# Kernel tuning notes

Hardware: AMD Instinct MI355X
Metric: run time of the kernel (lower is better)

The kernel has to match this reference:

```python
import jax, jax.numpy as jnp
import numpy as np

DIM = 1536
NUM_HEADS = 12
HEAD_DIM = DIM // NUM_HEADS  # 128
EPS = 1e-6


def _rms_norm(x, weight, eps=EPS):
    # x: [B, S, C], computed in float32 like the torch module
    xf = x.astype(jnp.float32)
    xf = xf * jax.lax.rsqrt(jnp.mean(xf * xf, axis=-1, keepdims=True) + eps)
    return (xf * weight).astype(x.dtype)


def _rotate_half(x):
    x1, x2 = jnp.split(x, 2, axis=-1)
    return jnp.concatenate([-x2, x1], axis=-1)


def setup_inputs() -> dict:
    key = jax.random.key(0)
    ks = jax.random.split(key, 12)
    B, S = 1, 4096
    scale = 1.0 / np.sqrt(DIM)
    x = jax.random.normal(ks[0], (B, S, DIM), dtype=jnp.float32)
    # RoPE tables [S, head_dim]
    pos = jnp.arange(S, dtype=jnp.float32)[:, None]
    inv_freq = 1.0 / (10000.0 ** (jnp.arange(0, HEAD_DIM, 2, dtype=jnp.float32) / HEAD_DIM))
    ang = pos * inv_freq[None, :]                      # [S, head_dim/2]
    ang = jnp.concatenate([ang, ang], axis=-1)         # [S, head_dim]
    freqs_cos = jnp.cos(ang)
    freqs_sin = jnp.sin(ang)
    Wq = jax.random.normal(ks[1], (DIM, DIM), dtype=jnp.float32) * scale
    bq = jnp.zeros((DIM,), dtype=jnp.float32)
    Wk = jax.random.normal(ks[2], (DIM, DIM), dtype=jnp.float32) * scale
    bk = jnp.zeros((DIM,), dtype=jnp.float32)
    Wv = jax.random.normal(ks[3], (DIM, DIM), dtype=jnp.float32) * scale
    bv = jnp.zeros((DIM,), dtype=jnp.float32)
    Wo = jax.random.normal(ks[4], (DIM, DIM), dtype=jnp.float32) * scale
    bo = jnp.zeros((DIM,), dtype=jnp.float32)
    gq = jnp.ones((DIM,), dtype=jnp.float32)
    gk = jnp.ones((DIM,), dtype=jnp.float32)
    return {"x": x, "freqs_cos": freqs_cos, "freqs_sin": freqs_sin,
            "Wq": Wq, "bq": bq, "Wk": Wk, "bk": bk, "Wv": Wv, "bv": bv,
            "Wo": Wo, "bo": bo, "gq": gq, "gk": gk}


def reference(x, freqs_cos, freqs_sin, Wq, bq, Wk, bk, Wv, bv, Wo, bo, gq, gk):
    b, s, _ = x.shape
    n, d = NUM_HEADS, HEAD_DIM
    q = _rms_norm(x @ Wq.T + bq, gq).reshape(b, s, n, d)
    k = _rms_norm(x @ Wk.T + bk, gk).reshape(b, s, n, d)
    v = (x @ Wv.T + bv).reshape(b, s, n, d)
    # RoPE: freqs [S, d] -> broadcast over batch and heads
    cos = freqs_cos[None, :, None, :]
    sin = freqs_sin[None, :, None, :]
    q = q * cos + _rotate_half(q) * sin
    k = k * cos + _rotate_half(k) * sin
    # SDPA, non-causal
    scores = jnp.einsum('bqnd,bknd->bnqk', q, k) / jnp.sqrt(jnp.asarray(d, x.dtype))
    attn = jax.nn.softmax(scores, axis=-1)
    out = jnp.einsum('bnqk,bknd->bqnd', attn, v).reshape(b, s, n * d)
    return out @ Wo.T + bo
```

## Files before the change

### kernel.cpp

```cpp
#include <hip/hip_runtime.h>

typedef unsigned short ushort_t;
typedef short bf16x8 __attribute__((ext_vector_type(8)));
typedef float f32x4 __attribute__((ext_vector_type(4)));
typedef float f32x16 __attribute__((ext_vector_type(16)));

#define S_LEN 4096
#define DIM   1536
#define NH    12
#define HD    128
#define KVSPLIT 4
#define ROWS (NH * S_LEN)
#define OPSPLIT_ELEMS ((size_t)ROWS * HD)

__device__ __forceinline__ float bf2f(ushort_t h) {
  union { unsigned u; float f; } v; v.u = ((unsigned)h) << 16; return v.f;
}
__device__ __forceinline__ ushort_t f2bf(float f) {
  union { float f; unsigned u; } v; v.f = f;
  return (ushort_t)((v.u + 0x7FFFu + ((v.u >> 16) & 1u)) >> 16);
}
__device__ __forceinline__ unsigned cvtpk(float lo, float hi_) {
  unsigned r; asm("v_cvt_pk_bf16_f32 %0, %1, %2" : "=v"(r) : "v"(lo), "v"(hi_)); return r;
}

#define GLD16(gp, lp) __builtin_amdgcn_global_load_lds( \
    (const __attribute__((address_space(1))) unsigned int*)(gp), \
    (__attribute__((address_space(3))) unsigned int*)(lp), 16, 0, 0)

__global__ void __launch_bounds__(256) cvt_bf16(const float* __restrict__ in,
                                                ushort_t* __restrict__ out, int n4) {
  int i = blockIdx.x * 256 + threadIdx.x;
  int stride = gridDim.x * 256;
  for (; i < n4; i += stride) {
    float4 v = ((const float4*)in)[i];
    ushort4 o;
    o.x = f2bf(v.x); o.y = f2bf(v.y); o.z = f2bf(v.z); o.w = f2bf(v.w);
    ((ushort4*)out)[i] = o;
  }
}

template <int F32OUT>
__global__ void __launch_bounds__(256) gemm_bt(
    const ushort_t* __restrict__ A, const ushort_t* __restrict__ Wbase,
    const float* __restrict__ b0, const float* __restrict__ b1, const float* __restrict__ b2,
    void* __restrict__ Cbase_v, int M, int N, int K)
{
  const int z = blockIdx.z;
  const ushort_t* W = Wbase + (size_t)z * N * K;
  const float* bias = (z == 0) ? b0 : (z == 1) ? b1 : b2;

  const int n0 = blockIdx.x * 128;
  const int m0 = blockIdx.y * 128;
  const int t = threadIdx.x;
  const int lane = t & 63;
  const int w = t >> 6;
  const int wr = w >> 1, wc = w & 1;
  const int mp = lane & 15, g = lane >> 4;

  __shared__ __attribute__((aligned(16))) ushort_t As[128 * 64];
  __shared__ __attribute__((aligned(16))) ushort_t Bs[128 * 64];

  f32x4 acc[4][4];
  f32x4 zero = {0.f, 0.f, 0.f, 0.f};
#pragma unroll
  for (int i = 0; i < 4; ++i)
#pragma unroll
    for (int j = 0; j < 4; ++j) acc[i][j] = zero;

  for (int kt = 0; kt < K; kt += 64) {
    __syncthreads();
#pragma unroll
    for (int i = 0; i < 4; ++i) {
      int p = i * 256 + t;
      int r = p >> 3, sl = p & 7;
      int sg = sl ^ (r & 7);
      GLD16(A + (size_t)(m0 + r) * K + kt + sg * 8, As + p * 8);
      GLD16(W + (size_t)(n0 + r) * K + kt + sg * 8, Bs + p * 8);
    }
    __syncthreads();
#pragma unroll
    for (int kk = 0; kk < 2; ++kk) {
      bf16x8 af[4], bfr[4];
#pragma unroll
      for (int mi = 0; mi < 4; ++mi) {
        int row = wr * 64 + mi * 16 + mp;
        int ch = (g + 4 * kk) ^ (row & 7);
        af[mi] = *(const bf16x8*)(As + row * 64 + ch * 8);
      }
#pragma unroll
      for (int ni = 0; ni < 4; ++ni) {
        int row = wc * 64 + ni * 16 + mp;
        int ch = (g + 4 * kk) ^ (row & 7);
        bfr[ni] = *(const bf16x8*)(Bs + row * 64 + ch * 8);
      }
#pragma unroll
      for (int mi = 0; mi < 4; ++mi)
#pragma unroll
        for (int ni = 0; ni < 4; ++ni)
          acc[mi][ni] = __builtin_amdgcn_mfma_f32_16x16x32_bf16(af[mi], bfr[ni], acc[mi][ni], 0, 0, 0);
    }
  }
#pragma unroll
  for (int ni = 0; ni < 4; ++ni) {
    int n = n0 + wc * 64 + ni * 16 + mp;
    float bv = bias[n];
#pragma unroll
    for (int mi = 0; mi < 4; ++mi) {
      int mbase = m0 + wr * 64 + mi * 16 + g * 4;
#pragma unroll
      for (int j = 0; j < 4; ++j) {
        if constexpr (F32OUT) {
          ((float*)Cbase_v)[(size_t)z * M * N + (size_t)(mbase + j) * N + n] =
              acc[mi][ni][j] + bv;
        } else {
          ((ushort_t*)Cbase_v)[(size_t)z * M * N + (size_t)(mbase + j) * N + n] =
              f2bf(acc[mi][ni][j] + bv);
        }
      }
    }
  }
}

__global__ void __launch_bounds__(256) epi_qkv(
    const ushort_t* __restrict__ raw,
    const float* __restrict__ gq, const float* __restrict__ gk,
    const float* __restrict__ fcos, const float* __restrict__ fsin,
    ushort_t* __restrict__ Qh, ushort_t* __restrict__ Kh, ushort_t* __restrict__ Vh)
{
  const int s = blockIdx.x;
  const int t = threadIdx.x;
  const ushort_t* rq = raw + (size_t)s * DIM;
  const ushort_t* rk = raw + (size_t)S_LEN * DIM + (size_t)s * DIM;
  const ushort_t* rv = raw + 2 * (size_t)S_LEN * DIM + (size_t)s * DIM;

  float sq = 0.f, sk = 0.f;
#pragma unroll
  for (int i = 0; i < 6; ++i) {
    int e = t + 256 * i;
    float a = bf2f(rq[e]); sq += a * a;
    float b = bf2f(rk[e]); sk += b * b;
  }
  for (int off = 1; off < 64; off <<= 1) {
    sq += __shfl_xor(sq, off, 64);
    sk += __shfl_xor(sk, off, 64);
  }
  __shared__ float red[2][4];
  int w = t >> 6;
  if ((t & 63) == 0) { red[0][w] = sq; red[1][w] = sk; }
  __syncthreads();
  sq = red[0][0] + red[0][1] + red[0][2] + red[0][3];
  sk = red[1][0] + red[1][1] + red[1][2] + red[1][3];
  float invq = rsqrtf(sq * (1.f / 1536.f) + 1e-6f);
  float invk = rsqrtf(sk * (1.f / 1536.f) + 1e-6f);

  const float qscale = 0.12752004708465604f;
#pragma unroll
  for (int i = 0; i < 3; ++i) {
    int p = t + 256 * i;
    int hh = p >> 6, d = p & 63;
    int e1 = hh * 128 + d, e2 = e1 + 64;
    float c1 = fcos[s * 128 + d],      s1 = fsin[s * 128 + d];
    float c2 = fcos[s * 128 + d + 64], s2 = fsin[s * 128 + d + 64];
    float q1 = bf2f(rq[e1]) * invq * gq[e1];
    float q2 = bf2f(rq[e2]) * invq * gq[e2];
    float k1 = bf2f(rk[e1]) * invk * gk[e1];
    float k2 = bf2f(rk[e2]) * invk * gk[e2];
    size_t ob = ((size_t)hh * S_LEN + s) * 128;
    Qh[ob + d]      = f2bf((q1 * c1 - q2 * s1) * qscale);
    Qh[ob + d + 64] = f2bf((q2 * c2 + q1 * s2) * qscale);
    Kh[ob + d]      = f2bf(k1 * c1 - k2 * s1);
    Kh[ob + d + 64] = f2bf(k2 * c2 + k1 * s2);
  }
#pragma unroll
  for (int i = 0; i < 6; ++i) {
    int e = t + 256 * i;
    int hh = e >> 7, d = e & 127;
    Vh[((size_t)hh * S_LEN + s) * 128 + d] = rv[e];
  }
}

__global__ void __launch_bounds__(256) transpose_v(const ushort_t* __restrict__ Vh,
                                                   ushort_t* __restrict__ VT) {
  const int st = blockIdx.x * 64;
  const int dt = blockIdx.y * 64;
  const int h = blockIdx.z;
  __shared__ ushort_t tile[64][65];
  const int t = threadIdx.x;
#pragma unroll
  for (int i = 0; i < 2; ++i) {
    int p = i * 256 + t;
    int r = p >> 3, c = (p & 7) * 8;
    bf16x8 v = *(const bf16x8*)(Vh + ((size_t)h * S_LEN + st + r) * 128 + dt + c);
#pragma unroll
    for (int j = 0; j < 8; ++j) tile[r][c + j] = ((ushort_t*)&v)[j];
  }
  __syncthreads();
#pragma unroll
  for (int i = 0; i < 2; ++i) {
    int p = i * 256 + t;
    int r = p >> 3, c = (p & 7) * 8;
    ushort_t tmp[8];
#pragma unroll
    for (int j = 0; j < 8; ++j) tmp[j] = tile[c + j][r];
    *(bf16x8*)(VT + ((size_t)h * 128 + dt + r) * S_LEN + st + c) = *(bf16x8*)tmp;
  }
}

__device__ __forceinline__ void stage_kv(const ushort_t* __restrict__ Kg,
                                         const ushort_t* __restrict__ Vg,
                                         ushort_t* KsB, ushort_t* VsB, int t) {
#pragma unroll
  for (int i = 0; i < 8; ++i) {
    int p = i * 128 + t;
    int r = p >> 4, sl = p & 15;
    int sg = sl ^ (r & 7);
    GLD16(Kg + (size_t)r * 128 + sg * 8, KsB + p * 8);
  }
#pragma unroll
  for (int i = 0; i < 8; ++i) {
    int p = i * 128 + t;
    int r = p >> 3, sl = p & 7;
    int sg = sl ^ (r & 7);
    GLD16(Vg + (size_t)r * S_LEN + sg * 8, VsB + p * 8);
  }
}

struct AttnState {
  f32x16 oacc[4];
  float mrun, lrun;
};

__device__ __forceinline__ void attn_tile(const ushort_t* KsB, const ushort_t* VsB,
                                          const bf16x8* qf, AttnState& st_,
                                          int ql, int hi) {
  f32x16 sa0, sa1;
#pragma unroll
  for (int r = 0; r < 16; ++r) { sa0[r] = 0.f; sa1[r] = 0.f; }
  __builtin_amdgcn_s_setprio(1);
#pragma unroll
  for (int s = 0; s < 8; ++s) {
    int ck = (2 * s + hi) ^ (ql & 7);
    bf16x8 k0 = *(const bf16x8*)(KsB + ql * 128 + ck * 8);
    bf16x8 k1 = *(const bf16x8*)(KsB + (32 + ql) * 128 + ck * 8);
    sa0 = __builtin_amdgcn_mfma_f32_32x32x16_bf16(k0, qf[s], sa0, 0, 0, 0);
    sa1 = __builtin_amdgcn_mfma_f32_32x32x16_bf16(k1, qf[s], sa1, 0, 0, 0);
  }
  __builtin_amdgcn_s_setprio(0);

  float mt[8];
#pragma unroll
  for (int r = 0; r < 8; ++r)
    mt[r] = fmaxf(fmaxf(sa0[r], sa0[r + 8]), fmaxf(sa1[r], sa1[r + 8]));
#pragma unroll
  for (int off = 4; off > 0; off >>= 1)
#pragma unroll
    for (int r = 0; r < 8; ++r)
      if (r < off) mt[r] = fmaxf(mt[r], mt[r + off]);
  float mx = fmaxf(mt[0], __shfl_xor(mt[0], 32));

  if (__any(mx - st_.mrun > 11.0f)) {
    float nm = fmaxf(st_.mrun, mx);
    float sc = exp2f(st_.mrun - nm);
    st_.mrun = nm;
    st_.lrun *= sc;
#pragma unroll
    for (int dt = 0; dt < 4; ++dt)
#pragma unroll
      for (int r = 0; r < 16; ++r) st_.oacc[dt][r] *= sc;
  }

  float rt[8];
#pragma unroll
  for (int r = 0; r < 16; ++r) {
    sa0[r] = exp2f(sa0[r] - st_.mrun);
    sa1[r] = exp2f(sa1[r] - st_.mrun);
  }
#pragma unroll
  for (int r = 0; r < 8; ++r) rt[r] = (sa0[r] + sa0[r + 8]) + (sa1[r] + sa1[r + 8]);
#pragma unroll
  for (int off = 4; off > 0; off >>= 1)
#pragma unroll
    for (int r = 0; r < 8; ++r)
      if (r < off) rt[r] += rt[r + off];
  st_.lrun += rt[0] + __shfl_xor(rt[0], 32);

  unsigned pw0[8], pw1[8];
#pragma unroll
  for (int a = 0; a < 4; ++a) {
    pw0[2 * a]     = cvtpk(sa0[4 * a], sa0[4 * a + 1]);
    pw0[2 * a + 1] = cvtpk(sa0[4 * a + 2], sa0[4 * a + 3]);
    pw1[2 * a]     = cvtpk(sa1[4 * a], sa1[4 * a + 1]);
    pw1[2 * a + 1] = cvtpk(sa1[4 * a + 2], sa1[4 * a + 3]);
  }

#pragma unroll
  for (int sx = 0; sx < 2; ++sx) {
#pragma unroll
    for (int ks = 0; ks < 2; ++ks) {
      unsigned q0w0 = sx ? pw1[4 * ks + 0] : pw0[4 * ks + 0];
      unsigned q0w1 = sx ? pw1[4 * ks + 1] : pw0[4 * ks + 1];
      unsigned q1w0 = sx ? pw1[4 * ks + 2] : pw0[4 * ks + 2];
      unsigned q1w1 = sx ? pw1[4 * ks + 3] : pw0[4 * ks + 3];
      unsigned sw0 = hi ? q0w0 : q1w0;
      unsigned sw1 = hi ? q0w1 : q1w1;
      unsigned rv0 = (unsigned)__shfl_xor((int)sw0, 32);
      unsigned rv1 = (unsigned)__shfl_xor((int)sw1, 32);
      union { unsigned u[4]; bf16x8 v; } fw;
      fw.u[0] = hi ? rv0 : q0w0;
      fw.u[1] = hi ? rv1 : q0w1;
      fw.u[2] = hi ? q1w0 : rv0;
      fw.u[3] = hi ? q1w1 : rv1;
      __builtin_amdgcn_s_setprio(1);
#pragma unroll
      for (int dt = 0; dt < 4; ++dt) {
        int d = 32 * dt + ql;
        int cv = (4 * sx + 2 * ks + hi) ^ (ql & 7);
        bf16x8 va = *(const bf16x8*)(VsB + d * 64 + cv * 8);
        st_.oacc[dt] = __builtin_amdgcn_mfma_f32_32x32x16_bf16(va, fw.v, st_.oacc[dt], 0, 0, 0);
      }
      __builtin_amdgcn_s_setprio(0);
    }
  }
}

__device__ __forceinline__ void attn_epilogue(AttnState& st_, int z, int row, int hi,
                                              ushort_t* __restrict__ opraw,
                                              ushort_t* __restrict__ opxb,
                                              float* __restrict__ mlbuf) {
  ushort_t* Op = (z < 3) ? (opraw + (size_t)z * OPSPLIT_ELEMS) : opxb;
  float inv = 1.f / st_.lrun;
#pragma unroll
  for (int dt = 0; dt < 4; ++dt) {
#pragma unroll
    for (int c = 0; c < 4; ++c) {
      float f0 = st_.oacc[dt][4 * c + 0] * inv, f1 = st_.oacc[dt][4 * c + 1] * inv;
      float f2 = st_.oacc[dt][4 * c + 2] * inv, f3 = st_.oacc[dt][4 * c + 3] * inv;
      uint2 u;
      u.x = cvtpk(f0, f1);
      u.y = cvtpk(f2, f3);
      *(uint2*)(Op + (size_t)row * 128 + 32 * dt + 8 * c + 4 * hi) = u;
    }
  }
  if (hi == 0) {
    mlbuf[2 * ((size_t)z * ROWS + row)]     = st_.mrun;
    mlbuf[2 * ((size_t)z * ROWS + row) + 1] = st_.lrun;
  }
}

__global__ void __launch_bounds__(128) attn32(
    const ushort_t* __restrict__ Qh, const ushort_t* __restrict__ Kh,
    const ushort_t* __restrict__ VT,
    ushort_t* __restrict__ opraw, ushort_t* __restrict__ opxb,
    float* __restrict__ mlbuf, int zoff)
{
  const int qt = blockIdx.x;
  const int h = blockIdx.y;
  const int z = blockIdx.z + zoff;
  const int t = threadIdx.x;
  const int lane = t & 63;
  const int w = t >> 6;
  const int ql = lane & 31;
  const int hi = lane >> 5;

  __shared__ __attribute__((aligned(16))) ushort_t Ks[64 * 128];
  __shared__ __attribute__((aligned(16))) ushort_t Vs[128 * 64];

  const int q0 = qt * 64 + w * 32;
  const size_t kbase = (size_t)h * S_LEN * 128;
  const size_t vbase = (size_t)h * 128 * S_LEN;

  bf16x8 qf[8];
#pragma unroll
  for (int s = 0; s < 8; ++s)
    qf[s] = *(const bf16x8*)(Qh + ((size_t)h * S_LEN + q0 + ql) * 128 + 16 * s + 8 * hi);

  AttnState st_;
#pragma unroll
  for (int dt = 0; dt < 4; ++dt)
#pragma unroll
    for (int r = 0; r < 16; ++r) st_.oacc[dt][r] = 0.f;
  st_.mrun = -1e30f; st_.lrun = 0.f;

  const int kvbeg = z * (S_LEN / KVSPLIT);
  const int kvend = kvbeg + S_LEN / KVSPLIT;
  for (int kv0 = kvbeg; kv0 < kvend; kv0 += 64) {
    __syncthreads();
    stage_kv(Kh + kbase + (size_t)kv0 * 128, VT + vbase + kv0, Ks, Vs, t);
    __syncthreads();
    attn_tile(Ks, Vs, qf, st_, ql, hi);
  }
  attn_epilogue(st_, z, h * S_LEN + q0 + ql, hi, opraw, opxb, mlbuf);
}

__global__ void __launch_bounds__(128) attn32p(
    const ushort_t* __restrict__ Qh, const ushort_t* __restrict__ Kh,
    const ushort_t* __restrict__ VT,
    ushort_t* __restrict__ opraw, ushort_t* __restrict__ opxb,
    float* __restrict__ mlbuf, int zoff)
{
  const int qt = blockIdx.x;
  const int h = blockIdx.y;
  const int z = blockIdx.z + zoff;
  const int t = threadIdx.x;
  const int lane = t & 63;
  const int w = t >> 6;
  const int ql = lane & 31;
  const int hi = lane >> 5;

  __shared__ __attribute__((aligned(16))) ushort_t Ks[2][64 * 128];
  __shared__ __attribute__((aligned(16))) ushort_t Vs[2][128 * 64];

  const int q0 = qt * 64 + w * 32;
  const size_t kbase = (size_t)h * S_LEN * 128;
  const size_t vbase = (size_t)h * 128 * S_LEN;

  bf16x8 qf[8];
#pragma unroll
  for (int s = 0; s < 8; ++s)
    qf[s] = *(const bf16x8*)(Qh + ((size_t)h * S_LEN + q0 + ql) * 128 + 16 * s + 8 * hi);

  AttnState st_;
#pragma unroll
  for (int dt = 0; dt < 4; ++dt)
#pragma unroll
    for (int r = 0; r < 16; ++r) st_.oacc[dt][r] = 0.f;
  st_.mrun = -1e30f; st_.lrun = 0.f;

  const int kvbeg = z * (S_LEN / KVSPLIT);
  const int NT = (S_LEN / KVSPLIT) / 64;

  stage_kv(Kh + kbase + (size_t)kvbeg * 128, VT + vbase + kvbeg, Ks[0], Vs[0], t);

  for (int it = 0; it < NT; ++it) {
    const int cur = it & 1;
    if (it + 1 < NT) {
      const int kvn = kvbeg + (it + 1) * 64;
      stage_kv(Kh + kbase + (size_t)kvn * 128, VT + vbase + kvn, Ks[cur ^ 1], Vs[cur ^ 1], t);
      asm volatile("s_waitcnt vmcnt(16)" ::: "memory");
    } else {
      asm volatile("s_waitcnt vmcnt(0)" ::: "memory");
    }
    __builtin_amdgcn_sched_barrier(0);
    __builtin_amdgcn_s_barrier();
    __builtin_amdgcn_sched_barrier(0);
    attn_tile(Ks[cur], Vs[cur], qf, st_, ql, hi);
    __builtin_amdgcn_s_barrier();
  }
  attn_epilogue(st_, z, h * S_LEN + q0 + ql, hi, opraw, opxb, mlbuf);
}

__global__ void __launch_bounds__(256) attn_combine(
    const ushort_t* __restrict__ opraw, const ushort_t* __restrict__ opxb,
    const float* __restrict__ mlbuf, ushort_t* __restrict__ hb)
{
  int gidx = blockIdx.x * 256 + threadIdx.x;
  int r = gidx >> 4;
  int c = gidx & 15;

  float m[KVSPLIT], l[KVSPLIT];
#pragma unroll
  for (int zz = 0; zz < KVSPLIT; ++zz) {
    m[zz] = mlbuf[2 * ((size_t)zz * ROWS + r)];
    l[zz] = mlbuf[2 * ((size_t)zz * ROWS + r) + 1];
  }
  float M = fmaxf(fmaxf(m[0], m[1]), fmaxf(m[2], m[3]));
  float wsum = 0.f, wz[KVSPLIT];
#pragma unroll
  for (int zz = 0; zz < KVSPLIT; ++zz) {
    wz[zz] = l[zz] * exp2f(m[zz] - M);
    wsum += wz[zz];
  }
  float invw = 1.f / wsum;

  float o[8];
#pragma unroll
  for (int j = 0; j < 8; ++j) o[j] = 0.f;
#pragma unroll
  for (int zz = 0; zz < KVSPLIT; ++zz) {
    const ushort_t* Op = (zz < 3) ? (opraw + (size_t)zz * OPSPLIT_ELEMS) : opxb;
    bf16x8 v = *(const bf16x8*)(Op + (size_t)r * 128 + c * 8);
#pragma unroll
    for (int j = 0; j < 8; ++j) o[j] += wz[zz] * bf2f((ushort_t)v[j]);
  }
  uint4 u;
  u.x = cvtpk(o[0] * invw, o[1] * invw);
  u.y = cvtpk(o[2] * invw, o[3] * invw);
  u.z = cvtpk(o[4] * invw, o[5] * invw);
  u.w = cvtpk(o[6] * invw, o[7] * invw);
  int q = r & (S_LEN - 1), h = r >> 12;
  *(uint4*)(hb + (size_t)q * DIM + h * 128 + c * 8) = u;
}

extern "C" void kernel_launch(void* const* d_in, const int* in_sizes, int n_in,
                              void* d_out, int out_size, void* d_ws, size_t ws_size,
                              hipStream_t stream) {
  const float* x    = (const float*)d_in[0];
  const float* fcos = (const float*)d_in[1];
  const float* fsin = (const float*)d_in[2];
  const float* Wq   = (const float*)d_in[3];
  const float* bq   = (const float*)d_in[4];
  const float* Wk   = (const float*)d_in[5];
  const float* bk   = (const float*)d_in[6];
  const float* Wv   = (const float*)d_in[7];
  const float* bv   = (const float*)d_in[8];
  const float* Wo   = (const float*)d_in[9];
  const float* bo   = (const float*)d_in[10];
  const float* gq   = (const float*)d_in[11];
  const float* gk   = (const float*)d_in[12];

  char* ws = (char*)d_ws;
  ushort_t* xb  = (ushort_t*)(ws);
  ushort_t* wb  = (ushort_t*)(ws + 12582912);
  ushort_t* raw = (ushort_t*)(ws + 31457280);
  ushort_t* Qh  = (ushort_t*)(ws + 69206016);
  ushort_t* Kh  = (ushort_t*)(ws + 81788928);
  ushort_t* Vh  = (ushort_t*)(ws + 94371840);
  ushort_t* VT  = (ushort_t*)(ws + 106954752);
  ushort_t* hb  = (ushort_t*)(ws + 119537664);

  cvt_bf16<<<2048, 256, 0, stream>>>(x,  xb,             6291456 / 4);
  cvt_bf16<<<2048, 256, 0, stream>>>(Wq, wb + 0 * 2359296, 2359296 / 4);
  cvt_bf16<<<2048, 256, 0, stream>>>(Wk, wb + 1 * 2359296, 2359296 / 4);
  cvt_bf16<<<2048, 256, 0, stream>>>(Wv, wb + 2 * 2359296, 2359296 / 4);
  cvt_bf16<<<2048, 256, 0, stream>>>(Wo, wb + 3 * 2359296, 2359296 / 4);

  gemm_bt<0><<<dim3(12, 32, 3), 256, 0, stream>>>(xb, wb, bq, bk, bv,
                                                  (void*)raw, 4096, 1536, 1536);
  epi_qkv<<<4096, 256, 0, stream>>>(raw, gq, gk, fcos, fsin, Qh, Kh, Vh);
  transpose_v<<<dim3(64, 2, 12), 256, 0, stream>>>(Vh, VT);

  attn32 <<<dim3(64, 12, 2), 128, 0, stream>>>(Qh, Kh, VT, raw, xb, (float*)Vh, 0);
  attn32p<<<dim3(64, 12, 2), 128, 0, stream>>>(Qh, Kh, VT, raw, xb, (float*)Vh, 2);

  attn_combine<<<3072, 256, 0, stream>>>(raw, xb, (const float*)Vh, hb);
  gemm_bt<1><<<dim3(12, 32, 1), 256, 0, stream>>>(hb, wb + 3 * 2359296, bo, bo, bo,
                                                  (void*)d_out, 4096, 1536, 1536);
}
```

Baseline: 536.0 us.

## Merge split attention launches into one 256-thread kernel with remapped block order

Replaces the two attention launches (one single-buffered, one double-buffered) with a single launch using 256-thread blocks that each cover 128 query rows, so each staged K/V tile is reused by four waves instead of two. Block IDs are remapped so consecutive blocks fall on different XCD slots, spreading heads and KV splits across the chip. This halves global K/V staging traffic per query and removes one launch. It also drops the double-buffered prefetch pipeline, so load latency is no longer overlapped with compute.

```diff
diff --git a/kernel.cpp b/kernel.cpp
--- a/kernel.cpp
+++ b/kernel.cpp
@@ -207,19 +207,19 @@
   }
 }
 
-__device__ __forceinline__ void stage_kv(const ushort_t* __restrict__ Kg,
-                                         const ushort_t* __restrict__ Vg,
-                                         ushort_t* KsB, ushort_t* VsB, int t) {
-#pragma unroll
-  for (int i = 0; i < 8; ++i) {
-    int p = i * 128 + t;
+__device__ __forceinline__ void stage_kv256(const ushort_t* __restrict__ Kg,
+                                            const ushort_t* __restrict__ Vg,
+                                            ushort_t* KsB, ushort_t* VsB, int t) {
+#pragma unroll
+  for (int i = 0; i < 4; ++i) {
+    int p = i * 256 + t;
     int r = p >> 4, sl = p & 15;
     int sg = sl ^ (r & 7);
     GLD16(Kg + (size_t)r * 128 + sg * 8, KsB + p * 8);
   }
 #pragma unroll
-  for (int i = 0; i < 8; ++i) {
-    int p = i * 128 + t;
+  for (int i = 0; i < 4; ++i) {
+    int p = i * 256 + t;
     int r = p >> 3, sl = p & 7;
     int sg = sl ^ (r & 7);
     GLD16(Vg + (size_t)r * S_LEN + sg * 8, VsB + p * 8);
@@ -348,15 +348,18 @@
   }
 }
 
-__global__ void __launch_bounds__(128) attn32(
+__global__ void __launch_bounds__(256) attn32(
     const ushort_t* __restrict__ Qh, const ushort_t* __restrict__ Kh,
     const ushort_t* __restrict__ VT,
     ushort_t* __restrict__ opraw, ushort_t* __restrict__ opxb,
-    float* __restrict__ mlbuf, int zoff)
+    float* __restrict__ mlbuf)
 {
-  const int qt = blockIdx.x;
-  const int h = blockIdx.y;
-  const int z = blockIdx.z + zoff;
+  int lid = blockIdx.x + 32 * (blockIdx.y + 12 * blockIdx.z);
+  int nid = (lid & 7) * 192 + (lid >> 3);
+  const int qt = nid & 31;
+  const int h = (nid >> 5) % NH;
+  const int z = nid / (32 * NH);
+
   const int t = threadIdx.x;
   const int lane = t & 63;
   const int w = t >> 6;
@@ -366,7 +369,7 @@
   __shared__ __attribute__((aligned(16))) ushort_t Ks[64 * 128];
   __shared__ __attribute__((aligned(16))) ushort_t Vs[128 * 64];
 
-  const int q0 = qt * 64 + w * 32;
+  const int q0 = qt * 128 + w * 32;
   const size_t kbase = (size_t)h * S_LEN * 128;
   const size_t vbase = (size_t)h * 128 * S_LEN;
 
@@ -386,66 +389,9 @@
   const int kvend = kvbeg + S_LEN / KVSPLIT;
   for (int kv0 = kvbeg; kv0 < kvend; kv0 += 64) {
     __syncthreads();
-    stage_kv(Kh + kbase + (size_t)kv0 * 128, VT + vbase + kv0, Ks, Vs, t);
+    stage_kv256(Kh + kbase + (size_t)kv0 * 128, VT + vbase + kv0, Ks, Vs, t);
     __syncthreads();
     attn_tile(Ks, Vs, qf, st_, ql, hi);
-  }
-  attn_epilogue(st_, z, h * S_LEN + q0 + ql, hi, opraw, opxb, mlbuf);
-}
-
-__global__ void __launch_bounds__(128) attn32p(
-    const ushort_t* __restrict__ Qh, const ushort_t* __restrict__ Kh,
-    const ushort_t* __restrict__ VT,
-    ushort_t* __restrict__ opraw, ushort_t* __restrict__ opxb,
-    float* __restrict__ mlbuf, int zoff)
-{
-  const int qt = blockIdx.x;
-  const int h = blockIdx.y;
-  const int z = blockIdx.z + zoff;
-  const int t = threadIdx.x;
-  const int lane = t & 63;
-  const int w = t >> 6;
-  const int ql = lane & 31;
-  const int hi = lane >> 5;
-
-  __shared__ __attribute__((aligned(16))) ushort_t Ks[2][64 * 128];
-  __shared__ __attribute__((aligned(16))) ushort_t Vs[2][128 * 64];
-
-  const int q0 = qt * 64 + w * 32;
-  const size_t kbase = (size_t)h * S_LEN * 128;
-  const size_t vbase = (size_t)h * 128 * S_LEN;
-
-  bf16x8 qf[8];
-#pragma unroll
-  for (int s = 0; s < 8; ++s)
-    qf[s] = *(const bf16x8*)(Qh + ((size_t)h * S_LEN + q0 + ql) * 128 + 16 * s + 8 * hi);
-
-  AttnState st_;
-#pragma unroll
-  for (int dt = 0; dt < 4; ++dt)
-#pragma unroll
-    for (int r = 0; r < 16; ++r) st_.oacc[dt][r] = 0.f;
-  st_.mrun = -1e30f; st_.lrun = 0.f;
-
-  const int kvbeg = z * (S_LEN / KVSPLIT);
-  const int NT = (S_LEN / KVSPLIT) / 64;
-
-  stage_kv(Kh + kbase + (size_t)kvbeg * 128, VT + vbase + kvbeg, Ks[0], Vs[0], t);
-
-  for (int it = 0; it < NT; ++it) {
-    const int cur = it & 1;
-    if (it + 1 < NT) {
-      const int kvn = kvbeg + (it + 1) * 64;
-      stage_kv(Kh + kbase + (size_t)kvn * 128, VT + vbase + kvn, Ks[cur ^ 1], Vs[cur ^ 1], t);
-      asm volatile("s_waitcnt vmcnt(16)" ::: "memory");
-    } else {
-      asm volatile("s_waitcnt vmcnt(0)" ::: "memory");
-    }
-    __builtin_amdgcn_sched_barrier(0);
-    __builtin_amdgcn_s_barrier();
-    __builtin_amdgcn_sched_barrier(0);
-    attn_tile(Ks[cur], Vs[cur], qf, st_, ql, hi);
-    __builtin_amdgcn_s_barrier();
   }
   attn_epilogue(st_, z, h * S_LEN + q0 + ql, hi, opraw, opxb, mlbuf);
 }
@@ -530,8 +476,7 @@
   epi_qkv<<<4096, 256, 0, stream>>>(raw, gq, gk, fcos, fsin, Qh, Kh, Vh);
   transpose_v<<<dim3(64, 2, 12), 256, 0, stream>>>(Vh, VT);
 
-  attn32 <<<dim3(64, 12, 2), 128, 0, stream>>>(Qh, Kh, VT, raw, xb, (float*)Vh, 0);
-  attn32p<<<dim3(64, 12, 2), 128, 0, stream>>>(Qh, Kh, VT, raw, xb, (float*)Vh, 2);
+  attn32<<<dim3(32, 12, KVSPLIT), 256, 0, stream>>>(Qh, Kh, VT, raw, xb, (float*)Vh);
 
   attn_combine<<<3072, 256, 0, stream>>>(raw, xb, (const float*)Vh, hb);
   gemm_bt<1><<<dim3(12, 32, 1), 256, 0, stream>>>(hb, wb + 3 * 2359296, bo, bo, bo,
```

Result: no change. 531.2 us (-0.9%).
